# Optimization experiments

Hardware: AMD Instinct MI355X
Metric: run time of the kernel (lower is better)

Reference implementation:

```python
import jax, jax.numpy as jnp
import numpy as np

VOCAB = 100000
EMBED = 128
BATCH = 64
INPUT_LEN = 128
NB_WORDS = 50
RETAIN_P = 1.0  # dropout = 0.0


def setup_inputs() -> dict:
    key = jax.random.key(0)
    k1, k2 = jax.random.split(key)
    X = jax.random.randint(k1, (BATCH, INPUT_LEN, NB_WORDS), 0, VOCAB, dtype=jnp.int32)
    W = jax.random.normal(k2, (VOCAB, EMBED), dtype=jnp.float32)
    # original build() zeroes row 0 (padding row)
    W = W.at[0].set(0.0)
    return {"X": X, "W": W}


def reference(X, W):
    # inference path: B = ones(input_dim) * retain_p, so W_eff = W * retain_p
    # gather: (B, L, nb_words, E)
    emb = W[X] * RETAIN_P
    # zero-mask padding index 0, then bag-of-words sum over word axis
    mask = (X != 0).astype(emb.dtype)[..., None]
    out = jnp.sum(emb * mask, axis=2)  # (B, L, E)
    return out
```

## Files before the change

### kernel.cpp

```cpp
#include <hip/hip_runtime.h>
#include <hip/hip_bf16.h>
#include <stdint.h>


#define VOCAB     100000
#define EMBED     128
#define BATCH     64
#define INPUT_LEN 128
#define NB_WORDS  50
#define POSITIONS (BATCH * INPUT_LEN)
#define W_ELEMS   (VOCAB * EMBED)

__device__ __forceinline__ uint32_t bf16_rne(float f) {
    uint32_t u = __builtin_bit_cast(uint32_t, f);
    return (u + 0x7fffu + ((u >> 16) & 1u)) >> 16;
}

__global__ __launch_bounds__(256) void w_to_bf16(
    const float* __restrict__ W,
    uint32_t* __restrict__ Wb)
{
    const int t = blockIdx.x * blockDim.x + threadIdx.x;
    const float4* __restrict__ W4 = (const float4*)W;
    float4 a = W4[(size_t)t * 2];
    float4 b = W4[(size_t)t * 2 + 1];
    uint4 o;
    o.x = bf16_rne(a.x) | (bf16_rne(a.y) << 16);
    o.y = bf16_rne(a.z) | (bf16_rne(a.w) << 16);
    o.z = bf16_rne(b.x) | (bf16_rne(b.y) << 16);
    o.w = bf16_rne(b.z) | (bf16_rne(b.w) << 16);
    ((uint4*)Wb)[t] = o;
}

__global__ __launch_bounds__(256, 8) void bag_gather_bf16(
    const int* __restrict__ X,
    const uint32_t* __restrict__ Wb,
    float* __restrict__ out)
{
    const int gtid = blockIdx.x * blockDim.x + threadIdx.x;
    const int pos  = gtid >> 6;
    const int lane = threadIdx.x & 63;

    const int* xp = X + pos * NB_WORDS;
    int myidx = (lane < NB_WORDS) ? xp[lane] : 0;

    uint32_t v[NB_WORDS];
    #pragma unroll
    for (int w = 0; w < NB_WORDS; ++w) {
        int idx = __shfl(myidx, w);
        v[w] = Wb[(size_t)idx * (EMBED / 2) + lane];
    }

    float accx = 0.0f, accy = 0.0f;
    #pragma unroll
    for (int w = 0; w < NB_WORDS; ++w) {
        accx += __builtin_bit_cast(float, v[w] << 16);
        accy += __builtin_bit_cast(float, v[w] & 0xffff0000u);
    }

    float2* o2 = (float2*)out;
    o2[(size_t)pos * (EMBED / 2) + lane] = make_float2(accx, accy);
}

__global__ __launch_bounds__(256) void bag_onephase(
    const int* __restrict__ X,
    const float* __restrict__ W,
    float* __restrict__ out)
{
    const int gtid = blockIdx.x * blockDim.x + threadIdx.x;
    const int pos  = gtid >> 6;
    const int lane = threadIdx.x & 63;
    if (pos >= POSITIONS) return;

    const int* xp = X + pos * NB_WORDS;
    int myidx = (lane < NB_WORDS) ? xp[lane] : 0;

    const float2* __restrict__ W2 = (const float2*)W;
    float2 acc = make_float2(0.0f, 0.0f);
    #pragma unroll
    for (int w = 0; w < NB_WORDS; ++w) {
        int idx = __shfl(myidx, w);
        float2 v = W2[(size_t)idx * (EMBED / 2) + lane];
        acc.x += v.x;
        acc.y += v.y;
    }
    float2* o2 = (float2*)out;
    o2[(size_t)pos * (EMBED / 2) + lane] = acc;
}

extern "C" void kernel_launch(void* const* d_in, const int* in_sizes, int n_in,
                              void* d_out, int out_size, void* d_ws, size_t ws_size,
                              hipStream_t stream) {
    const int*   X = (const int*)d_in[0];
    const float* W = (const float*)d_in[1];
    float*     out = (float*)d_out;

    const size_t ws_needed = (size_t)W_ELEMS * 2;
    if (ws_size >= ws_needed) {
        uint32_t* Wb = (uint32_t*)d_ws;
        w_to_bf16<<<W_ELEMS / 8 / 256, 256, 0, stream>>>(W, Wb);
        bag_gather_bf16<<<POSITIONS * 64 / 256, 256, 0, stream>>>(X, Wb, out);
    } else {
        bag_onephase<<<POSITIONS * 64 / 256, 256, 0, stream>>>(X, W, out);
    }
}
```

Measured before the change: 102.7 us.

## Partition vocab by XCD range so each XCD's L2 holds its slice of the table

Splits the vocabulary into 8 row ranges mapped to blockIdx&7, presumably to pin each range to one XCD so its bf16 slice of the table stays resident in that XCD's L2. Phase 1 has each block gather only the indices in its range, using ballot and readlane, and writes bf16 partial sums. Phase 2 reduces the 8 partials into fp32 output. The conversion kernel is reorganised the same way, with nontemporal loads. The cost is an extra kernel launch, an 8x larger partial-sum buffer to write and read back, bf16 rounding of the partials, and each position's X row being read 8 times.

After: 122.7 us. +19.5%, slower.

```diff
diff --git a/kernel.cpp b/kernel.cpp
--- a/kernel.cpp
+++ b/kernel.cpp
@@ -3,33 +3,111 @@
 #include <stdint.h>
 
 
-#define VOCAB     100000
-#define EMBED     128
-#define BATCH     64
-#define INPUT_LEN 128
-#define NB_WORDS  50
-#define POSITIONS (BATCH * INPUT_LEN)
-#define W_ELEMS   (VOCAB * EMBED)
+#define VOCAB          100000
+#define EMBED          128
+#define NB_WORDS       50
+#define POSITIONS      8192
+#define RANGES         8
+#define ROWS_PER_RANGE (VOCAB / RANGES)
+#define W_ELEMS        (VOCAB * EMBED)
+#define RANGE_ELEMS    (ROWS_PER_RANGE * EMBED)
+#define RANGE_CHUNKS   (RANGE_ELEMS / 8)
+#define CONV_BPR       ((RANGE_CHUNKS + 255) / 256)
+
+typedef float    f32x4 __attribute__((ext_vector_type(4)));
+typedef uint32_t u32x4 __attribute__((ext_vector_type(4)));
 
 __device__ __forceinline__ uint32_t bf16_rne(float f) {
     uint32_t u = __builtin_bit_cast(uint32_t, f);
     return (u + 0x7fffu + ((u >> 16) & 1u)) >> 16;
 }
+__device__ __forceinline__ uint32_t pack_bf16x2(float a, float b) {
+    return bf16_rne(a) | (bf16_rne(b) << 16);
+}
 
-__global__ __launch_bounds__(256) void w_to_bf16(
+__global__ __launch_bounds__(256) void w_to_bf16_xcd(
     const float* __restrict__ W,
     uint32_t* __restrict__ Wb)
 {
+    const int r = blockIdx.x & (RANGES - 1);
+    const int t = (blockIdx.x >> 3) * 256 + threadIdx.x;
+    if (t >= RANGE_CHUNKS) return;
+    const f32x4* __restrict__ W4 = (const f32x4*)W;
+    const size_t s = (size_t)r * (RANGE_CHUNKS * 2) + (size_t)t * 2;
+    f32x4 a = __builtin_nontemporal_load(&W4[s]);
+    f32x4 b = __builtin_nontemporal_load(&W4[s + 1]);
+    u32x4 o;
+    o.x = pack_bf16x2(a.x, a.y);
+    o.y = pack_bf16x2(a.z, a.w);
+    o.z = pack_bf16x2(b.x, b.y);
+    o.w = pack_bf16x2(b.z, b.w);
+    ((u32x4*)Wb)[(size_t)r * RANGE_CHUNKS + t] = o;
+}
+
+__global__ __launch_bounds__(256) void bag_phase1(
+    const int* __restrict__ X,
+    const uint32_t* __restrict__ Wb,
+    uint32_t* __restrict__ part)
+{
+    const int r    = blockIdx.x & (RANGES - 1);
+    const int pos  = (blockIdx.x >> 3) * 4 + (threadIdx.x >> 6);
+    const int lane = threadIdx.x & 63;
+    const int lo = r * ROWS_PER_RANGE;
+    const int hi = lo + ROWS_PER_RANGE;
+
+    int myidx = (lane < NB_WORDS)
+              ? __builtin_nontemporal_load(X + pos * NB_WORDS + lane) : -1;
+    unsigned long long m = __ballot(myidx >= lo && myidx < hi);
+
+    float ax = 0.0f, ay = 0.0f;
+    while (m) {
+        int id[8];
+        #pragma unroll
+        for (int j = 0; j < 8; ++j) {
+            if (m) {
+                int l = __ffsll((long long)m) - 1;
+                id[j] = __builtin_amdgcn_readlane(myidx, l);
+                m &= m - 1;
+            } else {
+                id[j] = 0;
+            }
+        }
+        uint32_t v[8];
+        #pragma unroll
+        for (int j = 0; j < 8; ++j)
+            v[j] = Wb[(size_t)id[j] * (EMBED / 2) + lane];
+        #pragma unroll
+        for (int j = 0; j < 8; ++j) {
+            ax += __builtin_bit_cast(float, v[j] << 16);
+            ay += __builtin_bit_cast(float, v[j] & 0xffff0000u);
+        }
+    }
+
+    __builtin_nontemporal_store(pack_bf16x2(ax, ay),
+        part + ((size_t)r * POSITIONS + pos) * (EMBED / 2) + lane);
+}
+
+__global__ __launch_bounds__(256) void bag_phase2(
+    const uint32_t* __restrict__ part,
+    float* __restrict__ out)
+{
     const int t = blockIdx.x * blockDim.x + threadIdx.x;
-    const float4* __restrict__ W4 = (const float4*)W;
-    float4 a = W4[(size_t)t * 2];
-    float4 b = W4[(size_t)t * 2 + 1];
-    uint4 o;
-    o.x = bf16_rne(a.x) | (bf16_rne(a.y) << 16);
-    o.y = bf16_rne(a.z) | (bf16_rne(a.w) << 16);
-    o.z = bf16_rne(b.x) | (bf16_rne(b.y) << 16);
-    o.w = bf16_rne(b.z) | (bf16_rne(b.w) << 16);
-    ((uint4*)Wb)[t] = o;
+    const u32x4* __restrict__ p4 = (const u32x4*)part;
+    float s[8] = {0.f, 0.f, 0.f, 0.f, 0.f, 0.f, 0.f, 0.f};
+    #pragma unroll
+    for (int r = 0; r < RANGES; ++r) {
+        u32x4 u = __builtin_nontemporal_load(
+            &p4[(size_t)r * POSITIONS * (EMBED / 8) + t]);
+        uint32_t ua[4] = {u.x, u.y, u.z, u.w};
+        #pragma unroll
+        for (int j = 0; j < 4; ++j) {
+            s[2 * j]     += __builtin_bit_cast(float, ua[j] << 16);
+            s[2 * j + 1] += __builtin_bit_cast(float, ua[j] & 0xffff0000u);
+        }
+    }
+    float4* o4 = (float4*)out;
+    o4[(size_t)t * 2]     = make_float4(s[0], s[1], s[2], s[3]);
+    o4[(size_t)t * 2 + 1] = make_float4(s[4], s[5], s[6], s[7]);
 }
 
 __global__ __launch_bounds__(256, 8) void bag_gather_bf16(
@@ -40,26 +118,21 @@
     const int gtid = blockIdx.x * blockDim.x + threadIdx.x;
     const int pos  = gtid >> 6;
     const int lane = threadIdx.x & 63;
-
     const int* xp = X + pos * NB_WORDS;
     int myidx = (lane < NB_WORDS) ? xp[lane] : 0;
-
     uint32_t v[NB_WORDS];
     #pragma unroll
     for (int w = 0; w < NB_WORDS; ++w) {
         int idx = __shfl(myidx, w);
         v[w] = Wb[(size_t)idx * (EMBED / 2) + lane];
     }
-
     float accx = 0.0f, accy = 0.0f;
     #pragma unroll
     for (int w = 0; w < NB_WORDS; ++w) {
         accx += __builtin_bit_cast(float, v[w] << 16);
         accy += __builtin_bit_cast(float, v[w] & 0xffff0000u);
     }
-
-    float2* o2 = (float2*)out;
-    o2[(size_t)pos * (EMBED / 2) + lane] = make_float2(accx, accy);
+    ((float2*)out)[(size_t)pos * (EMBED / 2) + lane] = make_float2(accx, accy);
 }
 
 __global__ __launch_bounds__(256) void bag_onephase(
@@ -70,22 +143,17 @@
     const int gtid = blockIdx.x * blockDim.x + threadIdx.x;
     const int pos  = gtid >> 6;
     const int lane = threadIdx.x & 63;
-    if (pos >= POSITIONS) return;
-
     const int* xp = X + pos * NB_WORDS;
     int myidx = (lane < NB_WORDS) ? xp[lane] : 0;
-
     const float2* __restrict__ W2 = (const float2*)W;
     float2 acc = make_float2(0.0f, 0.0f);
     #pragma unroll
     for (int w = 0; w < NB_WORDS; ++w) {
         int idx = __shfl(myidx, w);
         float2 v = W2[(size_t)idx * (EMBED / 2) + lane];
-        acc.x += v.x;
-        acc.y += v.y;
+        acc.x += v.x; acc.y += v.y;
     }
-    float2* o2 = (float2*)out;
-    o2[(size_t)pos * (EMBED / 2) + lane] = acc;
+    ((float2*)out)[(size_t)pos * (EMBED / 2) + lane] = acc;
 }
 
 extern "C" void kernel_launch(void* const* d_in, const int* in_sizes, int n_in,
@@ -95,10 +163,18 @@
     const float* W = (const float*)d_in[1];
     float*     out = (float*)d_out;
 
-    const size_t ws_needed = (size_t)W_ELEMS * 2;
-    if (ws_size >= ws_needed) {
+    const size_t wb_bytes   = (size_t)W_ELEMS * 2;
+    const size_t part_bytes = (size_t)RANGES * POSITIONS * EMBED * 2;
+
+    if (ws_size >= wb_bytes + part_bytes) {
+        uint32_t* Wb   = (uint32_t*)d_ws;
+        uint32_t* part = (uint32_t*)((char*)d_ws + wb_bytes);
+        w_to_bf16_xcd<<<RANGES * CONV_BPR, 256, 0, stream>>>(W, Wb);
+        bag_phase1<<<(POSITIONS / 4) * RANGES, 256, 0, stream>>>(X, Wb, part);
+        bag_phase2<<<POSITIONS * (EMBED / 8) / 256, 256, 0, stream>>>(part, out);
+    } else if (ws_size >= wb_bytes) {
         uint32_t* Wb = (uint32_t*)d_ws;
-        w_to_bf16<<<W_ELEMS / 8 / 256, 256, 0, stream>>>(W, Wb);
+        w_to_bf16_xcd<<<RANGES * CONV_BPR, 256, 0, stream>>>(W, Wb);
         bag_gather_bf16<<<POSITIONS * 64 / 256, 256, 0, stream>>>(X, Wb, out);
     } else {
         bag_onephase<<<POSITIONS * 64 / 256, 256, 0, stream>>>(X, W, out);
```
